# Kernel tuning notes

Measured on AMD Instinct MI355X. Metric: run time of the kernel, lower is better.

The kernel has to match this reference:

```python
import jax, jax.numpy as jnp
import numpy as np

HEAD_DIM = 32
KERNEL = 3
DILATION = 2
PAD = DILATION * (KERNEL - 1) // 2  # 'same' padding for dilated window
SCALE = HEAD_DIM ** -0.5


def _unfold_windows(x):
    """x: [B, d, H, W] -> [B, d, k*k, H, W] dilated local windows.
    Matches torch nn.Unfold ordering: kernel row-major (i outer, j inner)."""
    B, d, H, W = x.shape
    xp = jnp.pad(x, ((0, 0), (0, 0), (PAD, PAD), (PAD, PAD)))
    taps = [xp[:, :, i * DILATION:i * DILATION + H, j * DILATION:j * DILATION + W]
            for i in range(KERNEL) for j in range(KERNEL)]  # fixed 9-tap loop
    return jnp.stack(taps, axis=2)


def setup_inputs() -> dict:
    key = jax.random.key(0)
    kq, kk, kv = jax.random.split(key, 3)
    shape = (16, 32, 128, 128)
    return {
        "q": jax.random.normal(kq, shape, dtype=jnp.float32),
        "k": jax.random.normal(kk, shape, dtype=jnp.float32),
        "v": jax.random.normal(kv, shape, dtype=jnp.float32),
    }


def reference(q, k, v):
    # k,v windows: [B, d, n, H, W] with n = kernel_size**2
    kw = _unfold_windows(k)
    vw = _unfold_windows(v)
    # per-pixel 1xN attention: scores [B, n, H, W]
    attn = jnp.einsum('bdhw,bdnhw->bnhw', q, kw) * SCALE
    attn = jax.nn.softmax(attn, axis=1)
    # weighted sum over window taps -> [B, d, H, W]
    return jnp.einsum('bnhw,bdnhw->bdhw', attn, vw)
```

## Files before the change

### kernel.cpp

```cpp
#include <hip/hip_runtime.h>


#define BB 16
#define HD 32
#define HH 128
#define WW 128
#define PLANE (HH * WW)
#define CHUNK 4

__global__ __launch_bounds__(256) void dilate_attn_kernel(
    const float* __restrict__ q,
    const float* __restrict__ k,
    const float* __restrict__ v,
    float* __restrict__ out)
{
    const int tid  = threadIdx.x;
    const int wv   = tid >> 6;
    const int lane = tid & 63;
    const int w2   = lane * 2;

    const int bid   = blockIdx.x;
    const int tile  = (bid & 7) * 64 + (bid >> 3);
    const int rowid = tile * 4 + wv;
    const int h = rowid & (HH - 1);
    const int b = rowid >> 7;

    const size_t base = (size_t)b * HD * PLANE + (size_t)h * WW;

    const bool hlo = (h >= 2), hhi = (h <= HH - 3);
    const int  roff[3] = { hlo ? -2 * WW : 0, 0, hhi ? 2 * WW : 0 };
    const bool rv[3]   = { hlo, true, hhi };

    const bool tvlo = (lane >= 1), tvhi = (lane <= 62);

    const int cql = tvlo ? w2 - 2 : 0;
    const int cqh = tvhi ? w2 + 2 : w2;

    const int im1 = (lane + 63) & 63;
    const int ip1 = (lane + 1) & 63;

    float Plo0[3] = {0,0,0}, Plo1[3] = {0,0,0};
    float Pce0[3] = {0,0,0}, Pce1[3] = {0,0,0};
    float Phi0[3] = {0,0,0}, Phi1[3] = {0,0,0};

    const float* qrow = q + base;
    const float* krow = k + base;

    for (int c = 0; c < HD; c += CHUNK) {
        float2 ql[CHUNK], qc[CHUNK], qh[CHUNK], kr[CHUNK][3];
        #pragma unroll
        for (int u = 0; u < CHUNK; ++u) {
            const size_t dp = (size_t)(c + u) * PLANE;
            ql[u] = *(const float2*)(qrow + dp + cql);
            qc[u] = *(const float2*)(qrow + dp + w2);
            qh[u] = *(const float2*)(qrow + dp + cqh);
            #pragma unroll
            for (int r = 0; r < 3; ++r)
                kr[u][r] = *(const float2*)(krow + dp + roff[r] + w2);
        }
        #pragma unroll
        for (int u = 0; u < CHUNK; ++u) {
            #pragma unroll
            for (int r = 0; r < 3; ++r) {
                Plo0[r] = fmaf(qh[u].x, kr[u][r].x, Plo0[r]);
                Plo1[r] = fmaf(qh[u].y, kr[u][r].y, Plo1[r]);
                Pce0[r] = fmaf(qc[u].x, kr[u][r].x, Pce0[r]);
                Pce1[r] = fmaf(qc[u].y, kr[u][r].y, Pce1[r]);
                Phi0[r] = fmaf(ql[u].x, kr[u][r].x, Phi0[r]);
                Phi1[r] = fmaf(ql[u].y, kr[u][r].y, Phi1[r]);
            }
        }
    }

    float s0[9], s1[9];
    #pragma unroll
    for (int r = 0; r < 3; ++r) {
        const float a0 = __shfl(Plo0[r], im1), a1 = __shfl(Plo1[r], im1);
        const float b0 = __shfl(Phi0[r], ip1), b1 = __shfl(Phi1[r], ip1);
        const bool vlo = rv[r] && tvlo, vhi = rv[r] && tvhi;
        s0[r * 3 + 0] = vlo ? a0 : 0.f;      s1[r * 3 + 0] = vlo ? a1 : 0.f;
        s0[r * 3 + 1] = rv[r] ? Pce0[r] : 0.f; s1[r * 3 + 1] = rv[r] ? Pce1[r] : 0.f;
        s0[r * 3 + 2] = vhi ? b0 : 0.f;      s1[r * 3 + 2] = vhi ? b1 : 0.f;
    }

    const float scale = 0.17677669529663687f;
    {
        float m0 = -3.4e38f, m1 = -3.4e38f;
        #pragma unroll
        for (int n = 0; n < 9; ++n) {
            s0[n] *= scale; m0 = fmaxf(m0, s0[n]);
            s1[n] *= scale; m1 = fmaxf(m1, s1[n]);
        }
        float sum0 = 0.f, sum1 = 0.f;
        #pragma unroll
        for (int n = 0; n < 9; ++n) {
            s0[n] = __expf(s0[n] - m0); sum0 += s0[n];
            s1[n] = __expf(s1[n] - m1); sum1 += s1[n];
        }
        const float i0 = 1.f / sum0, i1 = 1.f / sum1;
        #pragma unroll
        for (int n = 0; n < 9; ++n) { s0[n] *= i0; s1[n] *= i1; }
    }

    #pragma unroll
    for (int r = 0; r < 3; ++r) {
        const bool vlo = rv[r] && tvlo, vhi = rv[r] && tvhi;
        if (!vlo)   { s0[r * 3 + 0] = 0.f; s1[r * 3 + 0] = 0.f; }
        if (!rv[r]) { s0[r * 3 + 1] = 0.f; s1[r * 3 + 1] = 0.f; }
        if (!vhi)   { s0[r * 3 + 2] = 0.f; s1[r * 3 + 2] = 0.f; }
    }

    float wl0[3], wl1[3], wh0[3], wh1[3], wc0[3], wc1[3];
    #pragma unroll
    for (int r = 0; r < 3; ++r) {
        const float a0 = __shfl(s0[r * 3 + 0], ip1), a1 = __shfl(s1[r * 3 + 0], ip1);
        const float b0 = __shfl(s0[r * 3 + 2], im1), b1 = __shfl(s1[r * 3 + 2], im1);
        wl0[r] = tvhi ? a0 : 0.f;  wl1[r] = tvhi ? a1 : 0.f;
        wh0[r] = tvlo ? b0 : 0.f;  wh1[r] = tvlo ? b1 : 0.f;
        wc0[r] = s0[r * 3 + 1];    wc1[r] = s1[r * 3 + 1];
    }

    const float* vrow = v + base;
    float*       orow = out + base;

    for (int c = 0; c < HD; c += CHUNK) {
        float2 vr[CHUNK][3];
        #pragma unroll
        for (int u = 0; u < CHUNK; ++u) {
            const size_t dp = (size_t)(c + u) * PLANE;
            #pragma unroll
            for (int r = 0; r < 3; ++r)
                vr[u][r] = *(const float2*)(vrow + dp + roff[r] + w2);
        }
        #pragma unroll
        for (int u = 0; u < CHUNK; ++u) {
            float tl0 = 0.f, tl1 = 0.f, tc0 = 0.f, tc1 = 0.f, th0 = 0.f, th1 = 0.f;
            #pragma unroll
            for (int r = 0; r < 3; ++r) {
                tl0 = fmaf(wl0[r], vr[u][r].x, tl0);
                tl1 = fmaf(wl1[r], vr[u][r].y, tl1);
                tc0 = fmaf(wc0[r], vr[u][r].x, tc0);
                tc1 = fmaf(wc1[r], vr[u][r].y, tc1);
                th0 = fmaf(wh0[r], vr[u][r].x, th0);
                th1 = fmaf(wh1[r], vr[u][r].y, th1);
            }
            const float rl0 = __shfl(tl0, im1), rl1 = __shfl(tl1, im1);
            const float rh0 = __shfl(th0, ip1), rh1 = __shfl(th1, ip1);
            *(float2*)(orow + (size_t)(c + u) * PLANE + w2) =
                make_float2(tc0 + rl0 + rh0, tc1 + rl1 + rh1);
        }
    }
}

extern "C" void kernel_launch(void* const* d_in, const int* in_sizes, int n_in,
                              void* d_out, int out_size, void* d_ws, size_t ws_size,
                              hipStream_t stream) {
    const float* q = (const float*)d_in[0];
    const float* k = (const float*)d_in[1];
    const float* v = (const float*)d_in[2];
    float* out = (float*)d_out;

    dim3 grid(BB * HH / 4);
    dim3 block(256);
    dilate_attn_kernel<<<grid, block, 0, stream>>>(q, k, v, out);
}
```

Baseline: 34.71 us.

## Split head dimension across waves with shared-memory score reduction

Each block now handles one image row, with its four waves each covering an 8-channel slice of the head dimension instead of one row per wave over all 32 channels. Partial q·k scores go through LDS, are summed across waves after a barrier, and each wave then applies softmax and does its own slice of the V accumulation. The grid grows fourfold and the dependent load chain per thread shortens, aiming for more memory-level parallelism. The cost is a block barrier, about 18KB of shared memory per block, and softmax computed redundantly in every wave.

```diff
diff --git a/kernel.cpp b/kernel.cpp
--- a/kernel.cpp
+++ b/kernel.cpp
@@ -6,26 +6,28 @@
 #define HH 128
 #define WW 128
 #define PLANE (HH * WW)
-#define CHUNK 4
+#define CHUNK 2
+#define DQ 8
 
-__global__ __launch_bounds__(256) void dilate_attn_kernel(
+__global__ __launch_bounds__(256, 6) void dilate_attn_kernel(
     const float* __restrict__ q,
     const float* __restrict__ k,
     const float* __restrict__ v,
     float* __restrict__ out)
 {
+    __shared__ float red[9 * 512];
+
     const int tid  = threadIdx.x;
     const int wv   = tid >> 6;
     const int lane = tid & 63;
     const int w2   = lane * 2;
 
     const int bid   = blockIdx.x;
-    const int tile  = (bid & 7) * 64 + (bid >> 3);
-    const int rowid = tile * 4 + wv;
+    const int rowid = (bid & 7) * 256 + (bid >> 3);
     const int h = rowid & (HH - 1);
     const int b = rowid >> 7;
 
-    const size_t base = (size_t)b * HD * PLANE + (size_t)h * WW;
+    const size_t dbase = ((size_t)b * HD + (size_t)wv * DQ) * PLANE + (size_t)h * WW;
 
     const bool hlo = (h >= 2), hhi = (h <= HH - 3);
     const int  roff[3] = { hlo ? -2 * WW : 0, 0, hhi ? 2 * WW : 0 };
@@ -39,14 +41,16 @@
     const int im1 = (lane + 63) & 63;
     const int ip1 = (lane + 1) & 63;
 
-    float Plo0[3] = {0,0,0}, Plo1[3] = {0,0,0};
-    float Pce0[3] = {0,0,0}, Pce1[3] = {0,0,0};
-    float Phi0[3] = {0,0,0}, Phi1[3] = {0,0,0};
+    float P[3][3][2];
+    #pragma unroll
+    for (int r = 0; r < 3; ++r)
+        #pragma unroll
+        for (int kd = 0; kd < 3; ++kd) { P[r][kd][0] = 0.f; P[r][kd][1] = 0.f; }
 
-    const float* qrow = q + base;
-    const float* krow = k + base;
+    const float* qrow = q + dbase;
+    const float* krow = k + dbase;
 
-    for (int c = 0; c < HD; c += CHUNK) {
+    for (int c = 0; c < DQ; c += CHUNK) {
         float2 ql[CHUNK], qc[CHUNK], qh[CHUNK], kr[CHUNK][3];
         #pragma unroll
         for (int u = 0; u < CHUNK; ++u) {
@@ -62,25 +66,48 @@
         for (int u = 0; u < CHUNK; ++u) {
             #pragma unroll
             for (int r = 0; r < 3; ++r) {
-                Plo0[r] = fmaf(qh[u].x, kr[u][r].x, Plo0[r]);
-                Plo1[r] = fmaf(qh[u].y, kr[u][r].y, Plo1[r]);
-                Pce0[r] = fmaf(qc[u].x, kr[u][r].x, Pce0[r]);
-                Pce1[r] = fmaf(qc[u].y, kr[u][r].y, Pce1[r]);
-                Phi0[r] = fmaf(ql[u].x, kr[u][r].x, Phi0[r]);
-                Phi1[r] = fmaf(ql[u].y, kr[u][r].y, Phi1[r]);
+                P[r][0][0] = fmaf(qh[u].x, kr[u][r].x, P[r][0][0]);
+                P[r][0][1] = fmaf(qh[u].y, kr[u][r].y, P[r][0][1]);
+                P[r][1][0] = fmaf(qc[u].x, kr[u][r].x, P[r][1][0]);
+                P[r][1][1] = fmaf(qc[u].y, kr[u][r].y, P[r][1][1]);
+                P[r][2][0] = fmaf(ql[u].x, kr[u][r].x, P[r][2][0]);
+                P[r][2][1] = fmaf(ql[u].y, kr[u][r].y, P[r][2][1]);
             }
+        }
+    }
+
+    #pragma unroll
+    for (int r = 0; r < 3; ++r)
+        #pragma unroll
+        for (int kd = 0; kd < 3; ++kd)
+            *(float2*)&red[(r * 3 + kd) * 512 + wv * 128 + w2] =
+                make_float2(P[r][kd][0], P[r][kd][1]);
+    __syncthreads();
+
+    float S[3][3][2];
+    #pragma unroll
+    for (int r = 0; r < 3; ++r) {
+        #pragma unroll
+        for (int kd = 0; kd < 3; ++kd) {
+            float ax = 0.f, ay = 0.f;
+            #pragma unroll
+            for (int w4 = 0; w4 < 4; ++w4) {
+                const float2 t = *(const float2*)&red[(r * 3 + kd) * 512 + w4 * 128 + w2];
+                ax += t.x; ay += t.y;
+            }
+            S[r][kd][0] = ax; S[r][kd][1] = ay;
         }
     }
 
     float s0[9], s1[9];
     #pragma unroll
     for (int r = 0; r < 3; ++r) {
-        const float a0 = __shfl(Plo0[r], im1), a1 = __shfl(Plo1[r], im1);
-        const float b0 = __shfl(Phi0[r], ip1), b1 = __shfl(Phi1[r], ip1);
+        const float a0 = __shfl(S[r][0][0], im1), a1 = __shfl(S[r][0][1], im1);
+        const float b0 = __shfl(S[r][2][0], ip1), b1 = __shfl(S[r][2][1], ip1);
         const bool vlo = rv[r] && tvlo, vhi = rv[r] && tvhi;
-        s0[r * 3 + 0] = vlo ? a0 : 0.f;      s1[r * 3 + 0] = vlo ? a1 : 0.f;
-        s0[r * 3 + 1] = rv[r] ? Pce0[r] : 0.f; s1[r * 3 + 1] = rv[r] ? Pce1[r] : 0.f;
-        s0[r * 3 + 2] = vhi ? b0 : 0.f;      s1[r * 3 + 2] = vhi ? b1 : 0.f;
+        s0[r * 3 + 0] = vlo ? a0 : 0.f;         s1[r * 3 + 0] = vlo ? a1 : 0.f;
+        s0[r * 3 + 1] = rv[r] ? S[r][1][0] : 0.f; s1[r * 3 + 1] = rv[r] ? S[r][1][1] : 0.f;
+        s0[r * 3 + 2] = vhi ? b0 : 0.f;         s1[r * 3 + 2] = vhi ? b1 : 0.f;
     }
 
     const float scale = 0.17677669529663687f;
@@ -120,10 +147,10 @@
         wc0[r] = s0[r * 3 + 1];    wc1[r] = s1[r * 3 + 1];
     }
 
-    const float* vrow = v + base;
-    float*       orow = out + base;
+    const float* vrow = v + dbase;
+    float*       orow = out + dbase;
 
-    for (int c = 0; c < HD; c += CHUNK) {
+    for (int c = 0; c < DQ; c += CHUNK) {
         float2 vr[CHUNK][3];
         #pragma unroll
         for (int u = 0; u < CHUNK; ++u) {
@@ -160,7 +187,7 @@
     const float* v = (const float*)d_in[2];
     float* out = (float*)d_out;
 
-    dim3 grid(BB * HH / 4);
+    dim3 grid(BB * HH);
     dim3 block(256);
     dilate_attn_kernel<<<grid, block, 0, stream>>>(q, k, v, out);
 }
```

Measured after the change: 41.94 us. +20.8%, slower.
